# Performance work log

Hardware: AMD Instinct MI355X
Metric: run time of the kernel (lower is better)

The kernel has to match this reference:

```python
import jax, jax.numpy as jnp
import numpy as np
from jax.scipy.stats import norm

N = 6144
D1, D2 = 3000, 1000
H = 128          # hardcoded hidden in VAEEncoder
LAT = 64
E = 16           # num_experts
K = 2            # top-k
NOISE_EPS = 0.01
BN_EPS = 1e-5


def setup_inputs() -> dict:
    key = jax.random.key(0)
    ks = jax.random.split(key, 24)
    xav = lambda k, i, o: jax.random.uniform(k, (i, o), jnp.float32,
                                             -np.sqrt(6.0 / (i + o)), np.sqrt(6.0 / (i + o)))
    u = jax.random.uniform(ks[0], (N, N), jnp.float32)
    adj = u / u.sum(axis=1, keepdims=True)  # row-normalized dense graph
    inp = {
        'x1': jax.random.normal(ks[1], (N, D1), jnp.float32),
        'x2': jax.random.normal(ks[2], (N, D2), jnp.float32),
        'adj': adj,
        # modality-1 VAE encoder
        'W1': xav(ks[3], D1, H), 'gamma1': jnp.ones((H,)), 'beta1': jnp.zeros((H,)),
        'Wmu1': xav(ks[4], H, LAT), 'bmu1': jnp.zeros((LAT,)),
        'Wlv1': xav(ks[5], H, LAT), 'blv1': jnp.zeros((LAT,)),
        # modality-2 VAE encoder
        'W2': xav(ks[6], D2, H), 'gamma2': jnp.ones((H,)), 'beta2': jnp.zeros((H,)),
        'Wmu2': xav(ks[7], H, LAT), 'bmu2': jnp.zeros((LAT,)),
        'Wlv2': xav(ks[8], H, LAT), 'blv2': jnp.zeros((LAT,)),
        # MoE gating (torch inits these to zero; small randn gives a non-degenerate baseline)
        'w_gate': 0.02 * jax.random.normal(ks[9], (LAT, E), jnp.float32),
        'w_noise': 0.02 * jax.random.normal(ks[10], (LAT, E), jnp.float32),
        # modality decoders
        'Wd1': xav(ks[11], LAT, LAT), 'Wfc1': xav(ks[12], LAT, D1), 'bfc1': jnp.zeros((D1,)),
        'Wd2': xav(ks[13], LAT, LAT), 'Wfc2': xav(ks[14], LAT, D2), 'bfc2': jnp.zeros((D2,)),
    }
    return inp


def _encode(x, adj, W, gamma, beta, Wmu, bmu, Wlv, blv):
    h = adj @ (x @ W)                                   # [N,H] GNN embed
    mu_b = h.mean(0)
    var_b = h.var(0)
    h = (h - mu_b) / jnp.sqrt(var_b + BN_EPS) * gamma + beta  # BatchNorm1d (train mode)
    return h @ Wmu + bmu, h @ Wlv + blv                 # mu, logvar [N,LAT]


def _cv_squared(v):
    return v.var(ddof=1) / (v.mean() ** 2 + 1e-10)


def _moe_gating(z, w_gate, w_noise, key):
    clean = z @ w_gate                                  # [N,E]
    std = jax.nn.softplus(z @ w_noise) + NOISE_EPS
    noisy = clean + jax.random.normal(key, clean.shape, clean.dtype) * std
    top_vals, top_idx = jax.lax.top_k(noisy, K + 1)     # [N,K+1]
    topk_gates = jax.nn.softmax(top_vals[:, :K], axis=1)
    rows = jnp.arange(z.shape[0])[:, None]
    gates = jnp.zeros_like(clean).at[rows, top_idx[:, :K]].set(topk_gates)
    # differentiable load estimate (prob each expert is in top-k)
    thr_in = top_vals[:, K][:, None]
    thr_out = top_vals[:, K - 1][:, None]
    is_in = noisy > thr_in
    prob = jnp.where(is_in, norm.cdf((clean - thr_in) / std), norm.cdf((clean - thr_out) / std))
    load = prob.sum(0)
    importance = gates.sum(0)
    loss = _cv_squared(importance) + _cv_squared(load)
    return gates, loss


def _decode(z, adj, Wd, Wfc, bfc):
    return (adj @ (z @ Wd)) @ Wfc + bfc                 # Decoder: mm, mm, Linear


def reference(x1, x2, adj,
              W1, gamma1, beta1, Wmu1, bmu1, Wlv1, blv1,
              W2, gamma2, beta2, Wmu2, bmu2, Wlv2, blv2,
              w_gate, w_noise,
              Wd1, Wfc1, bfc1, Wd2, Wfc2, bfc2):
    mu1, lv1 = _encode(x1, adj, W1, gamma1, beta1, Wmu1, bmu1, Wlv1, blv1)
    mu2, lv2 = _encode(x2, adj, W2, gamma2, beta2, Wmu2, bmu2, Wlv2, blv2)
    # Product of Experts over the 2 modalities
    mus = jnp.stack([mu1, mu2], 0)
    lvs = jnp.stack([lv1, lv2], 0)
    var = jnp.exp(lvs) + 1e-8
    T = 1.0 / (var + 1e-8)
    pd_mu = (mus * T).sum(0) / T.sum(0)
    pd_logvar = jnp.log(1.0 / T.sum(0) + 1e-8)
    z = pd_mu
    gates, moe_loss = _moe_gating(z, w_gate, w_noise, jax.random.key(42))
    recon1 = _decode(z, adj, Wd1, Wfc1, bfc1)
    recon2 = _decode(z, adj, Wd2, Wfc2, bfc2)
    return recon1, recon2, pd_mu, pd_logvar, gates, moe_loss
```

## Files before the change

### kernel.cpp

```cpp
#include <hip/hip_runtime.h>
#include <math.h>

#define NR    6144
#define DIM1  3000
#define DIM2  1000
#define HID   128
#define LATD  64
#define NEXP  16

typedef __bf16 bf16x8 __attribute__((ext_vector_type(8)));
typedef float  f32x4  __attribute__((ext_vector_type(4)));

__device__ __forceinline__ unsigned short f2bf_rne(float x) {
  unsigned u = __float_as_uint(x);
  u += 0x7FFFu + ((u >> 16) & 1u);
  return (unsigned short)(u >> 16);
}
__device__ __forceinline__ void split2(float v, unsigned short& h, unsigned short& l) {
  h = f2bf_rne(v);
  float hf = __uint_as_float((unsigned)h << 16);
  l = f2bf_rne(v - hf);
}
__device__ __forceinline__ unsigned cvt_pk_bf16(float a, float b) {
  unsigned r;
  asm("v_cvt_pk_bf16_f32 %0, %1, %2" : "=v"(r) : "v"(a), "v"(b));
  return r;
}

template<bool SPLIT3, bool ATOMIC>
__device__ __forceinline__ void gemm_body3(
    unsigned short* __restrict__ bufA,
    unsigned short* __restrict__ bufB0, unsigned short* __restrict__ bufB1,
    const float* __restrict__ A, const unsigned short* __restrict__ Bblk,
    const float* __restrict__ bias,
    float* __restrict__ C, int N, int lda, int ldc,
    int bm, int bn, int k0, int kend)
{
  const int tid  = threadIdx.x;
  const int lane = tid & 63;
  const int wave = tid >> 6;
  const int wm = wave >> 1, wn = wave & 1;
  const int lrow = lane & 15, kg = lane >> 4;
  const int nsteps = (kend - k0 + 31) >> 5;
  if (nsteps <= 0) return;

  f32x4 acc[4][4];
  #pragma unroll
  for (int f = 0; f < 4; ++f)
    #pragma unroll
    for (int g = 0; g < 4; ++g)
      #pragma unroll
      for (int j = 0; j < 4; ++j) acc[f][g][j] = 0.f;

  const int srow = tid >> 1;
  const int ks   = (tid & 1) * 16;
  const int s0   = (tid & 1) * 2;
  const float* aRow = A + (size_t)(bm + srow) * lda;
  const int rx = srow & 7;
  const int wa0 = srow * 64 + (((s0 + 0) ^ rx) * 8);
  const int wa1 = srow * 64 + (((s0 + 1) ^ rx) * 8);
  const int wa2 = srow * 64 + (((s0 + 4) ^ rx) * 8);
  const int wa3 = srow * 64 + (((s0 + 5) ^ rx) * 8);

  float va[16];

  #define LOAD_A(gk) {                                                  \
    const int kb = (gk) + ks;                                           \
    if (kb + 16 <= kend) {                                              \
      const float4* ap = (const float4*)(aRow + kb);                    \
      float4 f0 = ap[0], f1 = ap[1], f2 = ap[2], f3 = ap[3];            \
      va[0]=f0.x; va[1]=f0.y; va[2]=f0.z; va[3]=f0.w;                   \
      va[4]=f1.x; va[5]=f1.y; va[6]=f1.z; va[7]=f1.w;                   \
      va[8]=f2.x; va[9]=f2.y; va[10]=f2.z; va[11]=f2.w;                 \
      va[12]=f3.x; va[13]=f3.y; va[14]=f3.z; va[15]=f3.w;               \
    } else {                                                            \
      _Pragma("unroll")                                                 \
      for (int i = 0; i < 16; ++i) va[i] = (kb + i < kend) ? aRow[kb + i] : 0.f; \
    }                                                                   \
  }

  #define STAGE_B(gk, dst) {                                            \
    const unsigned short* _src = Bblk + ((size_t)((gk) >> 5)) * 8192 + wave * 2048 + lane * 8; \
    unsigned short* _d = (dst) + wave * 2048;                           \
    __builtin_amdgcn_global_load_lds((const __attribute__((address_space(1))) unsigned int*)(_src),        (__attribute__((address_space(3))) unsigned int*)(_d),        16, 0, 0); \
    __builtin_amdgcn_global_load_lds((const __attribute__((address_space(1))) unsigned int*)(_src + 512),  (__attribute__((address_space(3))) unsigned int*)(_d + 512),  16, 0, 0); \
    __builtin_amdgcn_global_load_lds((const __attribute__((address_space(1))) unsigned int*)(_src + 1024), (__attribute__((address_space(3))) unsigned int*)(_d + 1024), 16, 0, 0); \
    __builtin_amdgcn_global_load_lds((const __attribute__((address_space(1))) unsigned int*)(_src + 1536), (__attribute__((address_space(3))) unsigned int*)(_d + 1536), 16, 0, 0); \
  }

  LOAD_A(k0);
  STAGE_B(k0, bufB0);

  for (int s = 0; s < nsteps; ++s) {
    unsigned short* bCur = (s & 1) ? bufB1 : bufB0;
    unsigned short* bNxt = (s & 1) ? bufB0 : bufB1;

    unsigned hw[8], lw[8];
    #pragma unroll
    for (int i = 0; i < 8; ++i) {
      hw[i] = cvt_pk_bf16(va[2*i], va[2*i+1]);
      if (SPLIT3) {
        const float h0 = __uint_as_float(hw[i] << 16);
        const float h1 = __uint_as_float(hw[i] & 0xFFFF0000u);
        lw[i] = cvt_pk_bf16(va[2*i] - h0, va[2*i+1] - h1);
      } else {
        lw[i] = 0;
      }
    }

    __syncthreads();
    *(uint4*)&bufA[wa0] = make_uint4(hw[0], hw[1], hw[2], hw[3]);
    *(uint4*)&bufA[wa1] = make_uint4(hw[4], hw[5], hw[6], hw[7]);
    if (SPLIT3) {
      *(uint4*)&bufA[wa2] = make_uint4(lw[0], lw[1], lw[2], lw[3]);
      *(uint4*)&bufA[wa3] = make_uint4(lw[4], lw[5], lw[6], lw[7]);
    }
    __syncthreads();

    if (s + 1 < nsteps) {
      LOAD_A(k0 + (s + 1) * 32);
      STAGE_B(k0 + (s + 1) * 32, bNxt);
    }

    bf16x8 afh[4], bfh[4], afl[4], bfl[4];
    #pragma unroll
    for (int f = 0; f < 4; ++f) {
      const int r = wm * 64 + f * 16 + lrow;
      afh[f] = *(const bf16x8*)&bufA[r * 64 + ((kg ^ (r & 7)) * 8)];
      if (SPLIT3) afl[f] = *(const bf16x8*)&bufA[r * 64 + (((4 + kg) ^ (r & 7)) * 8)];
      const int n = wn * 64 + f * 16 + lrow;
      bfh[f] = *(const bf16x8*)&bCur[n * 64 + ((kg ^ (n & 7)) * 8)];
      if (SPLIT3) bfl[f] = *(const bf16x8*)&bCur[n * 64 + (((4 + kg) ^ (n & 7)) * 8)];
    }
    #pragma unroll
    for (int f = 0; f < 4; ++f)
      #pragma unroll
      for (int g = 0; g < 4; ++g) {
        acc[f][g] = __builtin_amdgcn_mfma_f32_16x16x32_bf16(afh[f], bfh[g], acc[f][g], 0, 0, 0);
        if constexpr (SPLIT3) {
          acc[f][g] = __builtin_amdgcn_mfma_f32_16x16x32_bf16(afl[f], bfh[g], acc[f][g], 0, 0, 0);
          acc[f][g] = __builtin_amdgcn_mfma_f32_16x16x32_bf16(afh[f], bfl[g], acc[f][g], 0, 0, 0);
        }
      }
  }
  #undef LOAD_A
  #undef STAGE_B

  #pragma unroll
  for (int f = 0; f < 4; ++f) {
    #pragma unroll
    for (int g = 0; g < 4; ++g) {
      const int row0 = bm + wm * 64 + f * 16 + (lane >> 4) * 4;
      const int col  = bn + wn * 64 + g * 16 + (lane & 15);
      if (col < N) {
        #pragma unroll
        for (int j = 0; j < 4; ++j) {
          const size_t idx = (size_t)(row0 + j) * ldc + col;
          if (ATOMIC) atomicAdd(&C[idx], acc[f][g][j]);
          else        C[idx] = acc[f][g][j] + (bias ? bias[col] : 0.f);
        }
      }
    }
  }
}

template<bool SPLIT3, bool ATOMIC>
__global__ __launch_bounds__(256, 3) void gemm_mfma3(
    const float* __restrict__ A, const unsigned short* __restrict__ Bblk,
    int kblocks_per_tile, const float* __restrict__ bias, float* __restrict__ C,
    int N, int lda, int ldc, int K, int kchunk)
{
  __shared__ alignas(16) unsigned short bufA[8192];
  __shared__ alignas(16) unsigned short bufB0[8192];
  __shared__ alignas(16) unsigned short bufB1[8192];
  const unsigned short* Bt = Bblk + (size_t)blockIdx.y * kblocks_per_tile * 8192;
  const int k0 = blockIdx.z * kchunk;
  gemm_body3<SPLIT3, ATOMIC>(bufA, bufB0, bufB1, A, Bt, bias, C, N, lda, ldc,
                             blockIdx.x * 128, blockIdx.y * 128, k0, min(k0 + kchunk, K));
}

__global__ __launch_bounds__(256, 3) void gemm_enc3(
    const float* __restrict__ x1, const unsigned short* __restrict__ W1blk,
    const float* __restrict__ x2, const unsigned short* __restrict__ W2blk,
    float* __restrict__ XW)
{
  __shared__ alignas(16) unsigned short bufA[8192];
  __shared__ alignas(16) unsigned short bufB0[8192];
  __shared__ alignas(16) unsigned short bufB1[8192];
  if (blockIdx.y == 0) {
    const int k0 = blockIdx.z * 384;
    gemm_body3<true, true>(bufA, bufB0, bufB1, x1, W1blk, nullptr, XW, HID, DIM1, 256,
                           blockIdx.x * 128, 0, k0, min(k0 + 384, DIM1));
  } else {
    const int k0 = blockIdx.z * 128;
    gemm_body3<true, true>(bufA, bufB0, bufB1, x2, W2blk, nullptr, XW + HID, HID, DIM2, 256,
                           blockIdx.x * 128, 0, k0, min(k0 + 128, DIM2));
  }
}

__global__ __launch_bounds__(256) void pack_b_blocks(
    const float* __restrict__ in, int K, int ldin, int Ncols, int col0,
    unsigned short* __restrict__ out)
{
  __shared__ unsigned short img[8192];
  const int tid = threadIdx.x;
  const int ks  = blockIdx.x;
  const int k0  = ks * 32;
  const int c   = tid & 127;
  const int h   = tid >> 7;
  const int colg = col0 + blockIdx.y * 128 + c;
  #pragma unroll
  for (int i = 0; i < 16; ++i) {
    const int kl = h + 2 * i;
    const int k  = k0 + kl;
    const float v = (k < K && colg < Ncols) ? in[(size_t)k * ldin + colg] : 0.f;
    unsigned short hi, lo;
    split2(v, hi, lo);
    const int base = c * 64 + (kl & 7);
    img[base + (((kl >> 3) ^ (c & 7)) * 8)]       = hi;
    img[base + ((((kl >> 3) + 4) ^ (c & 7)) * 8)] = lo;
  }
  __syncthreads();
  const size_t ob = ((size_t)blockIdx.y * gridDim.x + ks) * 8192;
  const uint4* s4 = (const uint4*)img;
  uint4* o4 = (uint4*)(out + ob);
  #pragma unroll
  for (int i = 0; i < 4; ++i) o4[tid + i * 256] = s4[tid + i * 256];
}

#define BM 64
#define BN 64
#define BK 16

__global__ __launch_bounds__(256) void gemm_f32(
    const float* __restrict__ A, const float* __restrict__ B,
    const float* __restrict__ bias, float* __restrict__ C,
    int M, int N, int K, int lda, int ldb, int ldc)
{
  __shared__ float At[BK][BM + 4];
  __shared__ float Bt[BK][BN + 4];
  const int tid = threadIdx.x;
  const int tx = tid & 15;
  const int ty = tid >> 4;
  const int bm = blockIdx.x * BM;
  const int bn = blockIdx.y * BN;

  float acc[4][4] = {};

  const int ar = tid >> 2;
  const int ak = (tid & 3) * 4;
  const int bk = tid >> 4;
  const int bc = (tid & 15) * 4;

  for (int k0 = 0; k0 < K; k0 += BK) {
    {
      float4 v = make_float4(0.f, 0.f, 0.f, 0.f);
      const int gr = bm + ar;
      const int gk = k0 + ak;
      if (gr < M && gk < K) {
        const float* p = &A[(size_t)gr * lda];
        if (gk + 3 < K) v = *reinterpret_cast<const float4*>(&p[gk]);
        else {
          v.x = p[gk];
          if (gk + 1 < K) v.y = p[gk + 1];
          if (gk + 2 < K) v.z = p[gk + 2];
        }
      }
      At[ak + 0][ar] = v.x; At[ak + 1][ar] = v.y;
      At[ak + 2][ar] = v.z; At[ak + 3][ar] = v.w;
    }
    {
      float4 v = make_float4(0.f, 0.f, 0.f, 0.f);
      const int gk = k0 + bk;
      const int gc = bn + bc;
      if (gk < K) {
        const float* p = &B[(size_t)gk * ldb];
        if (gc + 3 < N) v = *reinterpret_cast<const float4*>(&p[gc]);
        else {
          if (gc     < N) v.x = p[gc];
          if (gc + 1 < N) v.y = p[gc + 1];
          if (gc + 2 < N) v.z = p[gc + 2];
        }
      }
      *reinterpret_cast<float4*>(&Bt[bk][bc]) = v;
    }
    __syncthreads();
    #pragma unroll
    for (int kk = 0; kk < BK; ++kk) {
      float4 a4 = *reinterpret_cast<const float4*>(&At[kk][ty * 4]);
      float4 b4 = *reinterpret_cast<const float4*>(&Bt[kk][tx * 4]);
      float av[4] = {a4.x, a4.y, a4.z, a4.w};
      float bv[4] = {b4.x, b4.y, b4.z, b4.w};
      #pragma unroll
      for (int i = 0; i < 4; ++i)
        #pragma unroll
        for (int j = 0; j < 4; ++j)
          acc[i][j] = fmaf(av[i], bv[j], acc[i][j]);
    }
    __syncthreads();
  }

  #pragma unroll
  for (int i = 0; i < 4; ++i) {
    const int row = bm + ty * 4 + i;
    if (row >= M) continue;
    #pragma unroll
    for (int j = 0; j < 4; ++j) {
      const int col = bn + tx * 4 + j;
      if (col < N) {
        float v = acc[i][j];
        if (bias) v += bias[col];
        C[(size_t)row * ldc + col] = v;
      }
    }
  }
}

__global__ __launch_bounds__(256) void bnstats_kernel(
    const float* __restrict__ H2, float* __restrict__ ssum, float* __restrict__ ssq)
{
  const int c = threadIdx.x;
  const int r0 = blockIdx.x * 12;
  float s = 0.f, q = 0.f;
  #pragma unroll
  for (int i = 0; i < 12; ++i) {
    float v = H2[(size_t)(r0 + i) * 256 + c];
    s += v;
    q = fmaf(v, v, q);
  }
  atomicAdd(&ssum[c], s);
  atomicAdd(&ssq[c], q);
}

__global__ __launch_bounds__(256) void mulv_kernel(
    const float* __restrict__ H2, const float* __restrict__ ssum, const float* __restrict__ ssq,
    const float* __restrict__ g1, const float* __restrict__ b1,
    const float* __restrict__ Wmu1, const float* __restrict__ bmu1,
    const float* __restrict__ Wlv1, const float* __restrict__ blv1,
    const float* __restrict__ g2, const float* __restrict__ b2,
    const float* __restrict__ Wmu2, const float* __restrict__ bmu2,
    const float* __restrict__ Wlv2, const float* __restrict__ blv2,
    float* __restrict__ pd_mu_out, float* __restrict__ pd_lv_out, float* __restrict__ z_out)
{
  __shared__ float hn[4][256];
  const int tid = threadIdx.x;
  const int r0 = blockIdx.x * 4;

  for (int idx = tid; idx < 1024; idx += 256) {
    const int rr = idx >> 8;
    const int c  = idx & 255;
    const float mean = ssum[c] * (1.0f / 6144.0f);
    const float var  = ssq[c] * (1.0f / 6144.0f) - mean * mean;
    const float rstd = 1.0f / sqrtf(var + 1e-5f);
    const float gamma = (c < HID) ? g1[c] : g2[c - HID];
    const float beta  = (c < HID) ? b1[c] : b2[c - HID];
    const float v = H2[(size_t)(r0 + rr) * 256 + c];
    hn[rr][c] = (v - mean) * rstd * gamma + beta;
  }
  __syncthreads();

  const int rr = tid >> 6;
  const int j  = tid & 63;
  float mu1 = bmu1[j], lv1 = blv1[j], mu2 = bmu2[j], lv2 = blv2[j];
  #pragma unroll 4
  for (int k = 0; k < HID; ++k) {
    const float h1 = hn[rr][k];
    const float h2 = hn[rr][HID + k];
    mu1 = fmaf(h1, Wmu1[k * LATD + j], mu1);
    lv1 = fmaf(h1, Wlv1[k * LATD + j], lv1);
    mu2 = fmaf(h2, Wmu2[k * LATD + j], mu2);
    lv2 = fmaf(h2, Wlv2[k * LATD + j], lv2);
  }
  const float var1 = expf(lv1) + 1e-8f;
  const float var2 = expf(lv2) + 1e-8f;
  const float T1 = 1.0f / (var1 + 1e-8f);
  const float T2 = 1.0f / (var2 + 1e-8f);
  const float denom = T1 + T2;
  const float pmu = (mu1 * T1 + mu2 * T2) / denom;
  const float plv = logf(1.0f / denom + 1e-8f);
  const size_t o = (size_t)(r0 + rr) * LATD + j;
  pd_mu_out[o] = pmu;
  pd_lv_out[o] = plv;
  z_out[o]     = pmu;
}

__device__ __forceinline__ unsigned rotl32(unsigned x, int r) {
  return (x << r) | (x >> (32 - r));
}

__device__ float threefry_normal(unsigned i) {
  const unsigned ks0 = 0u;
  const unsigned ks1 = 42u;
  const unsigned ks2 = 0x1BD11BDAu ^ 0u ^ 42u;
  unsigned x0 = 0u + ks0;
  unsigned x1 = i + ks1;

  #define TF_ROUND(r) { x0 += x1; x1 = rotl32(x1, r); x1 ^= x0; }
  TF_ROUND(13) TF_ROUND(15) TF_ROUND(26) TF_ROUND(6)
  x0 += ks1; x1 += ks2 + 1u;
  TF_ROUND(17) TF_ROUND(29) TF_ROUND(16) TF_ROUND(24)
  x0 += ks2; x1 += ks0 + 2u;
  TF_ROUND(13) TF_ROUND(15) TF_ROUND(26) TF_ROUND(6)
  x0 += ks0; x1 += ks1 + 3u;
  TF_ROUND(17) TF_ROUND(29) TF_ROUND(16) TF_ROUND(24)
  x0 += ks1; x1 += ks2 + 4u;
  TF_ROUND(13) TF_ROUND(15) TF_ROUND(26) TF_ROUND(6)
  x0 += ks2; x1 += ks0 + 5u;
  #undef TF_ROUND

  const unsigned bits = x0 ^ x1;

  const unsigned fb = (bits >> 9) | 0x3F800000u;
  const float u01 = __uint_as_float(fb) - 1.0f;
  const float minval = -0.99999994f;
  float u = fmaf(u01, 2.0f, minval);
  u = fmaxf(minval, u);

  float w = -log1pf(-u * u);
  float p;
  if (w < 5.0f) {
    w = w - 2.5f;
    p = 2.81022636e-08f;
    p = fmaf(p, w, 3.43273939e-07f);
    p = fmaf(p, w, -3.5233877e-06f);
    p = fmaf(p, w, -4.39150654e-06f);
    p = fmaf(p, w, 0.00021858087f);
    p = fmaf(p, w, -0.00125372503f);
    p = fmaf(p, w, -0.00417768164f);
    p = fmaf(p, w, 0.246640727f);
    p = fmaf(p, w, 1.50140941f);
  } else {
    w = sqrtf(w) - 3.0f;
    p = -0.000200214257f;
    p = fmaf(p, w, 0.000100950558f);
    p = fmaf(p, w, 0.00134934322f);
    p = fmaf(p, w, -0.00367342844f);
    p = fmaf(p, w, 0.00573950773f);
    p = fmaf(p, w, -0.0076224613f);
    p = fmaf(p, w, 0.00943887047f);
    p = fmaf(p, w, 1.00167406f);
    p = fmaf(p, w, 2.83297682f);
  }
  return 1.4142135f * (p * u);
}

__global__ __launch_bounds__(64) void gating_kernel(
    const float* __restrict__ z, const float* __restrict__ w_gate,
    const float* __restrict__ w_noise, float* __restrict__ gates_out,
    float* __restrict__ importance, float* __restrict__ loadv)
{
  __shared__ float zt[64][65];
  __shared__ float wg[64][16];
  __shared__ float wn[64][16];
  __shared__ float imp_s[16];
  __shared__ float load_s[16];

  const int tid = threadIdx.x;
  const int r0 = blockIdx.x * 64;

  for (int idx = tid; idx < 1024; idx += 64) {
    wg[idx >> 4][idx & 15] = w_gate[idx];
    wn[idx >> 4][idx & 15] = w_noise[idx];
  }
  for (int idx = tid; idx < 4096; idx += 64) {
    const int rr = idx >> 6, c = idx & 63;
    zt[rr][c] = z[(size_t)(r0 + rr) * 64 + c];
  }
  if (tid < 16) { imp_s[tid] = 0.f; load_s[tid] = 0.f; }
  __syncthreads();

  const int r = r0 + tid;
  float clean[16], noisy[16], stdv[16];
  #pragma unroll
  for (int e = 0; e < NEXP; ++e) {
    float c = 0.f, n = 0.f;
    #pragma unroll 8
    for (int k = 0; k < 64; ++k) {
      const float zv = zt[tid][k];
      c = fmaf(zv, wg[k][e], c);
      n = fmaf(zv, wn[k][e], n);
    }
    clean[e] = c;
    const float sp = fmaxf(n, 0.f) + log1pf(expf(-fabsf(n)));
    stdv[e] = sp + 0.01f;
    const float eps = threefry_normal((unsigned)r * 16u + (unsigned)e);
    noisy[e] = fmaf(eps, stdv[e], c);
  }

  float v0 = -1e30f, v1 = -1e30f, v2 = -1e30f;
  int i0 = 0, i1 = 0;
  #pragma unroll
  for (int e = 0; e < NEXP; ++e) {
    const float v = noisy[e];
    if (v > v0)      { v2 = v1; v1 = v0; i1 = i0; v0 = v; i0 = e; }
    else if (v > v1) { v2 = v1; v1 = v; i1 = e; }
    else if (v > v2) { v2 = v; }
  }

  const float e1 = expf(v1 - v0);
  const float inv = 1.0f / (1.0f + e1);
  const float g0 = inv;
  const float g1v = e1 * inv;

  float lacc[16];
  #pragma unroll
  for (int e = 0; e < NEXP; ++e) {
    const float gv = (e == i0) ? g0 : ((e == i1) ? g1v : 0.f);
    gates_out[(size_t)r * NEXP + e] = gv;
    const float thr = (noisy[e] > v2) ? v2 : v1;
    const float x = (clean[e] - thr) / stdv[e];
    lacc[e] = 0.5f * erfcf(-0.70710678f * x);
  }
  atomicAdd(&imp_s[i0], g0);
  atomicAdd(&imp_s[i1], g1v);
  #pragma unroll
  for (int e = 0; e < NEXP; ++e) atomicAdd(&load_s[e], lacc[e]);
  __syncthreads();
  if (tid < 16) {
    atomicAdd(&importance[tid], imp_s[tid]);
    atomicAdd(&loadv[tid], load_s[tid]);
  }
}

__global__ void loss_kernel(const float* __restrict__ imp, const float* __restrict__ ld,
                            float* __restrict__ out)
{
  if (threadIdx.x == 0 && blockIdx.x == 0) {
    float mi = 0.f, ml = 0.f;
    for (int e = 0; e < NEXP; ++e) { mi += imp[e]; ml += ld[e]; }
    mi *= (1.0f / 16.0f);
    ml *= (1.0f / 16.0f);
    float vi = 0.f, vl = 0.f;
    for (int e = 0; e < NEXP; ++e) {
      const float di = imp[e] - mi;
      const float dl = ld[e] - ml;
      vi = fmaf(di, di, vi);
      vl = fmaf(dl, dl, vl);
    }
    vi *= (1.0f / 15.0f);
    vl *= (1.0f / 15.0f);
    out[0] = vi / (mi * mi + 1e-10f) + vl / (ml * ml + 1e-10f);
  }
}

extern "C" void kernel_launch(void* const* d_in, const int* in_sizes, int n_in,
                              void* d_out, int out_size, void* d_ws, size_t ws_size,
                              hipStream_t stream)
{
  const float* x1     = (const float*)d_in[0];
  const float* x2     = (const float*)d_in[1];
  const float* adj    = (const float*)d_in[2];
  const float* W1     = (const float*)d_in[3];
  const float* gamma1 = (const float*)d_in[4];
  const float* beta1  = (const float*)d_in[5];
  const float* Wmu1   = (const float*)d_in[6];
  const float* bmu1   = (const float*)d_in[7];
  const float* Wlv1   = (const float*)d_in[8];
  const float* blv1   = (const float*)d_in[9];
  const float* W2     = (const float*)d_in[10];
  const float* gamma2 = (const float*)d_in[11];
  const float* beta2  = (const float*)d_in[12];
  const float* Wmu2   = (const float*)d_in[13];
  const float* bmu2   = (const float*)d_in[14];
  const float* Wlv2   = (const float*)d_in[15];
  const float* blv2   = (const float*)d_in[16];
  const float* w_gate = (const float*)d_in[17];
  const float* w_noise= (const float*)d_in[18];
  const float* Wd1    = (const float*)d_in[19];
  const float* Wfc1   = (const float*)d_in[20];
  const float* bfc1   = (const float*)d_in[21];
  const float* Wd2    = (const float*)d_in[22];
  const float* Wfc2   = (const float*)d_in[23];
  const float* bfc2   = (const float*)d_in[24];

  float* out = (float*)d_out;
  float* recon1 = out;
  float* recon2 = out + (size_t)NR * DIM1;
  float* pd_mu  = recon2 + (size_t)NR * DIM2;
  float* pd_lv  = pd_mu + (size_t)NR * LATD;
  float* gates  = pd_lv + (size_t)NR * LATD;
  float* loss   = gates + (size_t)NR * NEXP;

  char* wsb = (char*)d_ws;
  const size_t o_XW   = 0;
  const size_t o_H2   = o_XW   + 6291456;
  const size_t o_z    = o_H2   + 6291456;
  const size_t o_ZD   = o_z    + 1572864;
  const size_t o_AZ   = o_ZD   + 3145728;
  const size_t o_XWB  = o_AZ   + 3145728;
  const size_t o_W1B  = o_XWB  + 6291456;
  const size_t o_W2B  = o_W1B  + 1540096;
  const size_t o_stat = o_W2B  + 524288;
  const size_t need   = o_stat + 2176;

  const dim3 blk(256);

  if (ws_size >= need) {
    float* XW   = (float*)(wsb + o_XW);
    float* H2   = (float*)(wsb + o_H2);
    float* zbuf = (float*)(wsb + o_z);
    float* ZD   = (float*)(wsb + o_ZD);
    float* AZ   = (float*)(wsb + o_AZ);
    unsigned short* XWB  = (unsigned short*)(wsb + o_XWB);
    unsigned short* ZDB  = XWB;
    unsigned short* W1B  = (unsigned short*)(wsb + o_W1B);
    unsigned short* W2B  = (unsigned short*)(wsb + o_W2B);
    unsigned short* F1B  = W1B;
    unsigned short* F2B  = W2B;
    float* ssum = (float*)(wsb + o_stat);
    float* ssq  = ssum + 256;
    float* imp  = ssq + 256;
    float* ldv  = imp + 16;

    hipMemsetAsync(XW, 0, 6291456 * 2, stream);
    hipMemsetAsync(AZ, 0, 3145728, stream);
    hipMemsetAsync(ssum, 0, 2176, stream);

    pack_b_blocks<<<dim3(94, 1), blk, 0, stream>>>(W1, DIM1, HID, HID, 0, W1B);
    pack_b_blocks<<<dim3(32, 1), blk, 0, stream>>>(W2, DIM2, HID, HID, 0, W2B);

    gemm_enc3<<<dim3(48, 2, 8), blk, 0, stream>>>(x1, W1B, x2, W2B, XW);

    pack_b_blocks<<<dim3(192, 2), blk, 0, stream>>>(XW, NR, 256, 256, 0, XWB);

    gemm_mfma3<true, true><<<dim3(48, 2, 8), blk, 0, stream>>>(
        adj, XWB, 192, nullptr, H2, 256, NR, 256, NR, 768);

    bnstats_kernel<<<512, blk, 0, stream>>>(H2, ssum, ssq);
    mulv_kernel<<<NR / 4, blk, 0, stream>>>(H2, ssum, ssq,
        gamma1, beta1, Wmu1, bmu1, Wlv1, blv1,
        gamma2, beta2, Wmu2, bmu2, Wlv2, blv2,
        pd_mu, pd_lv, zbuf);

    gating_kernel<<<NR / 64, 64, 0, stream>>>(zbuf, w_gate, w_noise, gates, imp, ldv);
    loss_kernel<<<1, 64, 0, stream>>>(imp, ldv, loss);

    gemm_f32<<<dim3(96, 1), blk, 0, stream>>>(zbuf, Wd1, nullptr, ZD,        NR, LATD, LATD, LATD, LATD, 128);
    gemm_f32<<<dim3(96, 1), blk, 0, stream>>>(zbuf, Wd2, nullptr, ZD + LATD, NR, LATD, LATD, LATD, LATD, 128);

    pack_b_blocks<<<dim3(192, 1), blk, 0, stream>>>(ZD, NR, 128, 128, 0, ZDB);
    gemm_mfma3<false, true><<<dim3(48, 1, 16), blk, 0, stream>>>(
        adj, ZDB, 192, nullptr, AZ, 128, NR, 128, NR, 384);

    pack_b_blocks<<<dim3(2, 24), blk, 0, stream>>>(Wfc1, LATD, DIM1, DIM1, 0, F1B);
    pack_b_blocks<<<dim3(2, 8),  blk, 0, stream>>>(Wfc2, LATD, DIM2, DIM2, 0, F2B);

    gemm_mfma3<false, false><<<dim3(48, 24, 1), blk, 0, stream>>>(
        AZ, F1B, 2, bfc1, recon1, DIM1, 128, DIM1, LATD, 64);
    gemm_mfma3<false, false><<<dim3(48, 8, 1), blk, 0, stream>>>(
        AZ + LATD, F2B, 2, bfc2, recon2, DIM2, 128, DIM2, LATD, 64);
    return;
  }

  float* ws   = (float*)d_ws;
  float* XW   = ws;
  float* H2   = ws + 1572864;
  float* zbuf = ws + 3145728;
  float* ZD   = ws + 3538944;
  float* AZ   = ws + 4325376;
  float* ssum = ws + 5111808;
  float* ssq  = ws + 5112064;
  float* imp  = ws + 5112320;
  float* ldv  = ws + 5112336;

  hipMemsetAsync(ssum, 0, 544 * sizeof(float), stream);

  gemm_f32<<<dim3(NR / BM, 2), blk, 0, stream>>>(x1, W1, nullptr, XW,        NR, HID, DIM1, DIM1, HID, 256);
  gemm_f32<<<dim3(NR / BM, 2), blk, 0, stream>>>(x2, W2, nullptr, XW + HID,  NR, HID, DIM2, DIM2, HID, 256);
  gemm_f32<<<dim3(NR / BM, 4), blk, 0, stream>>>(adj, XW, nullptr, H2, NR, 256, NR, NR, 256, 256);
  bnstats_kernel<<<512, blk, 0, stream>>>(H2, ssum, ssq);
  mulv_kernel<<<NR / 4, blk, 0, stream>>>(H2, ssum, ssq,
                                          gamma1, beta1, Wmu1, bmu1, Wlv1, blv1,
                                          gamma2, beta2, Wmu2, bmu2, Wlv2, blv2,
                                          pd_mu, pd_lv, zbuf);
  gating_kernel<<<NR / 64, 64, 0, stream>>>(zbuf, w_gate, w_noise, gates, imp, ldv);
  loss_kernel<<<1, 64, 0, stream>>>(imp, ldv, loss);
  gemm_f32<<<dim3(NR / BM, 1), blk, 0, stream>>>(zbuf, Wd1, nullptr, ZD,        NR, LATD, LATD, LATD, LATD, 128);
  gemm_f32<<<dim3(NR / BM, 1), blk, 0, stream>>>(zbuf, Wd2, nullptr, ZD + LATD, NR, LATD, LATD, LATD, LATD, 128);
  gemm_f32<<<dim3(NR / BM, 2), blk, 0, stream>>>(adj, ZD, nullptr, AZ, NR, 128, NR, NR, 128, 128);
  gemm_f32<<<dim3(NR / BM, (DIM1 + BN - 1) / BN), blk, 0, stream>>>(AZ,        Wfc1, bfc1, recon1, NR, DIM1, LATD, 128, DIM1, DIM1);
  gemm_f32<<<dim3(NR / BM, (DIM2 + BN - 1) / BN), blk, 0, stream>>>(AZ + LATD, Wfc2, bfc2, recon2, NR, DIM2, LATD, 128, DIM2, DIM2);
}
```

Before: 431.2 us.

## Pack B operands in MFMA fragment order and load directly to registers

Replaces the tile-shaped B packing and LDS double-buffered staging with a fragment-ordered packed layout that each wave reads straight from global memory into registers. This removes two 16 KB LDS buffers per block and the associated LDS reads. It allows more occupancy, at the cost of losing the async prefetch overlap for B and exposing global load latency inside the loop. The A path still goes through LDS as before.

```diff
diff --git a/kernel.cpp b/kernel.cpp
--- a/kernel.cpp
+++ b/kernel.cpp
@@ -28,10 +28,10 @@
 }
 
 template<bool SPLIT3, bool ATOMIC>
-__device__ __forceinline__ void gemm_body3(
+__device__ __forceinline__ void gemm_bodyD(
     unsigned short* __restrict__ bufA,
-    unsigned short* __restrict__ bufB0, unsigned short* __restrict__ bufB1,
-    const float* __restrict__ A, const unsigned short* __restrict__ Bblk,
+    const float* __restrict__ A,
+    const unsigned short* __restrict__ Bpk, int nks, int ntile0,
     const float* __restrict__ bias,
     float* __restrict__ C, int N, int lda, int ldc,
     int bm, int bn, int k0, int kend)
@@ -61,6 +61,9 @@
   const int wa1 = srow * 64 + (((s0 + 1) ^ rx) * 8);
   const int wa2 = srow * 64 + (((s0 + 4) ^ rx) * 8);
   const int wa3 = srow * 64 + (((s0 + 5) ^ rx) * 8);
+
+  const unsigned short* pBbase =
+      Bpk + ((size_t)(ntile0 + wn * 4) * nks + (k0 >> 5)) * 1024 + lane * 8;
 
   float va[16];
 
@@ -79,22 +82,9 @@
     }                                                                   \
   }
 
-  #define STAGE_B(gk, dst) {                                            \
-    const unsigned short* _src = Bblk + ((size_t)((gk) >> 5)) * 8192 + wave * 2048 + lane * 8; \
-    unsigned short* _d = (dst) + wave * 2048;                           \
-    __builtin_amdgcn_global_load_lds((const __attribute__((address_space(1))) unsigned int*)(_src),        (__attribute__((address_space(3))) unsigned int*)(_d),        16, 0, 0); \
-    __builtin_amdgcn_global_load_lds((const __attribute__((address_space(1))) unsigned int*)(_src + 512),  (__attribute__((address_space(3))) unsigned int*)(_d + 512),  16, 0, 0); \
-    __builtin_amdgcn_global_load_lds((const __attribute__((address_space(1))) unsigned int*)(_src + 1024), (__attribute__((address_space(3))) unsigned int*)(_d + 1024), 16, 0, 0); \
-    __builtin_amdgcn_global_load_lds((const __attribute__((address_space(1))) unsigned int*)(_src + 1536), (__attribute__((address_space(3))) unsigned int*)(_d + 1536), 16, 0, 0); \
-  }
-
   LOAD_A(k0);
-  STAGE_B(k0, bufB0);
 
   for (int s = 0; s < nsteps; ++s) {
-    unsigned short* bCur = (s & 1) ? bufB1 : bufB0;
-    unsigned short* bNxt = (s & 1) ? bufB0 : bufB1;
-
     unsigned hw[8], lw[8];
     #pragma unroll
     for (int i = 0; i < 8; ++i) {
@@ -117,20 +107,22 @@
     }
     __syncthreads();
 
-    if (s + 1 < nsteps) {
-      LOAD_A(k0 + (s + 1) * 32);
-      STAGE_B(k0 + (s + 1) * 32, bNxt);
-    }
-
-    bf16x8 afh[4], bfh[4], afl[4], bfl[4];
+    bf16x8 bfh[4], bfl[4];
+    #pragma unroll
+    for (int g = 0; g < 4; ++g) {
+      const unsigned short* p = pBbase + ((size_t)g * nks + s) * 1024;
+      bfh[g] = *(const bf16x8*)p;
+      if (SPLIT3) bfl[g] = *(const bf16x8*)(p + 512);
+    }
+
+    if (s + 1 < nsteps) { LOAD_A(k0 + (s + 1) * 32); }
+
+    bf16x8 afh[4], afl[4];
     #pragma unroll
     for (int f = 0; f < 4; ++f) {
       const int r = wm * 64 + f * 16 + lrow;
       afh[f] = *(const bf16x8*)&bufA[r * 64 + ((kg ^ (r & 7)) * 8)];
       if (SPLIT3) afl[f] = *(const bf16x8*)&bufA[r * 64 + (((4 + kg) ^ (r & 7)) * 8)];
-      const int n = wn * 64 + f * 16 + lrow;
-      bfh[f] = *(const bf16x8*)&bCur[n * 64 + ((kg ^ (n & 7)) * 8)];
-      if (SPLIT3) bfl[f] = *(const bf16x8*)&bCur[n * 64 + (((4 + kg) ^ (n & 7)) * 8)];
     }
     #pragma unroll
     for (int f = 0; f < 4; ++f)
@@ -144,7 +136,6 @@
       }
   }
   #undef LOAD_A
-  #undef STAGE_B
 
   #pragma unroll
   for (int f = 0; f < 4; ++f) {
@@ -165,67 +156,63 @@
 }
 
 template<bool SPLIT3, bool ATOMIC>
-__global__ __launch_bounds__(256, 3) void gemm_mfma3(
-    const float* __restrict__ A, const unsigned short* __restrict__ Bblk,
-    int kblocks_per_tile, const float* __restrict__ bias, float* __restrict__ C,
+__global__ __launch_bounds__(256, 3) void gemm_mfmaD(
+    const float* __restrict__ A, const unsigned short* __restrict__ Bpk,
+    int nks, const float* __restrict__ bias, float* __restrict__ C,
     int N, int lda, int ldc, int K, int kchunk)
 {
   __shared__ alignas(16) unsigned short bufA[8192];
-  __shared__ alignas(16) unsigned short bufB0[8192];
-  __shared__ alignas(16) unsigned short bufB1[8192];
-  const unsigned short* Bt = Bblk + (size_t)blockIdx.y * kblocks_per_tile * 8192;
   const int k0 = blockIdx.z * kchunk;
-  gemm_body3<SPLIT3, ATOMIC>(bufA, bufB0, bufB1, A, Bt, bias, C, N, lda, ldc,
-                             blockIdx.x * 128, blockIdx.y * 128, k0, min(k0 + kchunk, K));
-}
-
-__global__ __launch_bounds__(256, 3) void gemm_enc3(
-    const float* __restrict__ x1, const unsigned short* __restrict__ W1blk,
-    const float* __restrict__ x2, const unsigned short* __restrict__ W2blk,
+  gemm_bodyD<SPLIT3, ATOMIC>(bufA, A, Bpk, nks, blockIdx.y * 8, bias, C,
+                             N, lda, ldc,
+                             blockIdx.x * 128, blockIdx.y * 128,
+                             k0, min(k0 + kchunk, K));
+}
+
+__global__ __launch_bounds__(256, 3) void gemm_encD(
+    const float* __restrict__ x1, const unsigned short* __restrict__ W1pk,
+    const float* __restrict__ x2, const unsigned short* __restrict__ W2pk,
     float* __restrict__ XW)
 {
   __shared__ alignas(16) unsigned short bufA[8192];
-  __shared__ alignas(16) unsigned short bufB0[8192];
-  __shared__ alignas(16) unsigned short bufB1[8192];
   if (blockIdx.y == 0) {
     const int k0 = blockIdx.z * 384;
-    gemm_body3<true, true>(bufA, bufB0, bufB1, x1, W1blk, nullptr, XW, HID, DIM1, 256,
+    gemm_bodyD<true, true>(bufA, x1, W1pk, 94, 0, nullptr, XW, HID, DIM1, 256,
                            blockIdx.x * 128, 0, k0, min(k0 + 384, DIM1));
   } else {
     const int k0 = blockIdx.z * 128;
-    gemm_body3<true, true>(bufA, bufB0, bufB1, x2, W2blk, nullptr, XW + HID, HID, DIM2, 256,
+    gemm_bodyD<true, true>(bufA, x2, W2pk, 32, 0, nullptr, XW + HID, HID, DIM2, 256,
                            blockIdx.x * 128, 0, k0, min(k0 + 128, DIM2));
   }
 }
 
-__global__ __launch_bounds__(256) void pack_b_blocks(
-    const float* __restrict__ in, int K, int ldin, int Ncols, int col0,
+__global__ __launch_bounds__(256) void pack_b_frags(
+    const float* __restrict__ in, int K, int ldin, int Ncols, int nks,
     unsigned short* __restrict__ out)
 {
-  __shared__ unsigned short img[8192];
-  const int tid = threadIdx.x;
-  const int ks  = blockIdx.x;
-  const int k0  = ks * 32;
-  const int c   = tid & 127;
-  const int h   = tid >> 7;
-  const int colg = col0 + blockIdx.y * 128 + c;
-  #pragma unroll
-  for (int i = 0; i < 16; ++i) {
-    const int kl = h + 2 * i;
-    const int k  = k0 + kl;
-    const float v = (k < K && colg < Ncols) ? in[(size_t)k * ldin + colg] : 0.f;
-    unsigned short hi, lo;
-    split2(v, hi, lo);
-    const int base = c * 64 + (kl & 7);
-    img[base + (((kl >> 3) ^ (c & 7)) * 8)]       = hi;
-    img[base + ((((kl >> 3) + 4) ^ (c & 7)) * 8)] = lo;
-  }
-  __syncthreads();
-  const size_t ob = ((size_t)blockIdx.y * gridDim.x + ks) * 8192;
-  const uint4* s4 = (const uint4*)img;
-  uint4* o4 = (uint4*)(out + ob);
-  #pragma unroll
-  for (int i = 0; i < 4; ++i) o4[tid + i * 256] = s4[tid + i * 256];
+  const int lane = threadIdx.x & 63;
+  const int sub  = threadIdx.x >> 6;
+  const int t = blockIdx.x;
+  const int s = blockIdx.y * 4 + sub;
+  if (s >= nks) return;
+  const int n  = t * 16 + (lane & 15);
+  const int kb = s * 32 + (lane >> 4) * 8;
+  const bool nv = (n < Ncols);
+  unsigned hw[4], lw[4];
+  #pragma unroll
+  for (int i = 0; i < 4; ++i) {
+    const int ka = kb + 2 * i, kc = ka + 1;
+    const float v0 = (nv && ka < K) ? in[(size_t)ka * ldin + n] : 0.f;
+    const float v1 = (nv && kc < K) ? in[(size_t)kc * ldin + n] : 0.f;
+    unsigned short h0, l0, h1, l1;
+    split2(v0, h0, l0);
+    split2(v1, h1, l1);
+    hw[i] = (unsigned)h0 | ((unsigned)h1 << 16);
+    lw[i] = (unsigned)l0 | ((unsigned)l1 << 16);
+  }
+  unsigned short* cell = out + ((size_t)t * nks + s) * 1024;
+  *(uint4*)(cell + lane * 8)       = make_uint4(hw[0], hw[1], hw[2], hw[3]);
+  *(uint4*)(cell + 512 + lane * 8) = make_uint4(lw[0], lw[1], lw[2], lw[3]);
 }
 
 #define BM 64
@@ -601,12 +588,12 @@
     float* zbuf = (float*)(wsb + o_z);
     float* ZD   = (float*)(wsb + o_ZD);
     float* AZ   = (float*)(wsb + o_AZ);
-    unsigned short* XWB  = (unsigned short*)(wsb + o_XWB);
-    unsigned short* ZDB  = XWB;
-    unsigned short* W1B  = (unsigned short*)(wsb + o_W1B);
-    unsigned short* W2B  = (unsigned short*)(wsb + o_W2B);
-    unsigned short* F1B  = W1B;
-    unsigned short* F2B  = W2B;
+    unsigned short* XWP = (unsigned short*)(wsb + o_XWB);
+    unsigned short* ZDP = XWP;
+    unsigned short* W1P = (unsigned short*)(wsb + o_W1B);
+    unsigned short* W2P = (unsigned short*)(wsb + o_W2B);
+    unsigned short* F1P = W1P;
+    unsigned short* F2P = W2P;
     float* ssum = (float*)(wsb + o_stat);
     float* ssq  = ssum + 256;
     float* imp  = ssq + 256;
@@ -616,15 +603,15 @@
     hipMemsetAsync(AZ, 0, 3145728, stream);
     hipMemsetAsync(ssum, 0, 2176, stream);
 
-    pack_b_blocks<<<dim3(94, 1), blk, 0, stream>>>(W1, DIM1, HID, HID, 0, W1B);
-    pack_b_blocks<<<dim3(32, 1), blk, 0, stream>>>(W2, DIM2, HID, HID, 0, W2B);
-
-    gemm_enc3<<<dim3(48, 2, 8), blk, 0, stream>>>(x1, W1B, x2, W2B, XW);
-
-    pack_b_blocks<<<dim3(192, 2), blk, 0, stream>>>(XW, NR, 256, 256, 0, XWB);
-
-    gemm_mfma3<true, true><<<dim3(48, 2, 8), blk, 0, stream>>>(
-        adj, XWB, 192, nullptr, H2, 256, NR, 256, NR, 768);
+    pack_b_frags<<<dim3(8, 24), blk, 0, stream>>>(W1, DIM1, HID, HID, 94, W1P);
+    pack_b_frags<<<dim3(8, 8),  blk, 0, stream>>>(W2, DIM2, HID, HID, 32, W2P);
+
+    gemm_encD<<<dim3(48, 2, 8), blk, 0, stream>>>(x1, W1P, x2, W2P, XW);
+
+    pack_b_frags<<<dim3(16, 48), blk, 0, stream>>>(XW, NR, 256, 256, 192, XWP);
+
+    gemm_mfmaD<true, true><<<dim3(48, 2, 8), blk, 0, stream>>>(
+        adj, XWP, 192, nullptr, H2, 256, NR, 256, NR, 768);
 
     bnstats_kernel<<<512, blk, 0, stream>>>(H2, ssum, ssq);
     mulv_kernel<<<NR / 4, blk, 0, stream>>>(H2, ssum, ssq,
@@ -638,17 +625,17 @@
     gemm_f32<<<dim3(96, 1), blk, 0, stream>>>(zbuf, Wd1, nullptr, ZD,        NR, LATD, LATD, LATD, LATD, 128);
     gemm_f32<<<dim3(96, 1), blk, 0, stream>>>(zbuf, Wd2, nullptr, ZD + LATD, NR, LATD, LATD, LATD, LATD, 128);
 
-    pack_b_blocks<<<dim3(192, 1), blk, 0, stream>>>(ZD, NR, 128, 128, 0, ZDB);
-    gemm_mfma3<false, true><<<dim3(48, 1, 16), blk, 0, stream>>>(
-        adj, ZDB, 192, nullptr, AZ, 128, NR, 128, NR, 384);
-
-    pack_b_blocks<<<dim3(2, 24), blk, 0, stream>>>(Wfc1, LATD, DIM1, DIM1, 0, F1B);
-    pack_b_blocks<<<dim3(2, 8),  blk, 0, stream>>>(Wfc2, LATD, DIM2, DIM2, 0, F2B);
-
-    gemm_mfma3<false, false><<<dim3(48, 24, 1), blk, 0, stream>>>(
-        AZ, F1B, 2, bfc1, recon1, DIM1, 128, DIM1, LATD, 64);
-    gemm_mfma3<false, false><<<dim3(48, 8, 1), blk, 0, stream>>>(
-        AZ + LATD, F2B, 2, bfc2, recon2, DIM2, 128, DIM2, LATD, 64);
+    pack_b_frags<<<dim3(8, 48), blk, 0, stream>>>(ZD, NR, 128, 128, 192, ZDP);
+    gemm_mfmaD<false, true><<<dim3(48, 1, 16), blk, 0, stream>>>(
+        adj, ZDP, 192, nullptr, AZ, 128, NR, 128, NR, 384);
+
+    pack_b_frags<<<dim3(192, 1), blk, 0, stream>>>(Wfc1, LATD, DIM1, DIM1, 2, F1P);
+    pack_b_frags<<<dim3(64, 1),  blk, 0, stream>>>(Wfc2, LATD, DIM2, DIM2, 2, F2P);
+
+    gemm_mfmaD<false, false><<<dim3(48, 24, 1), blk, 0, stream>>>(
+        AZ, F1P, 2, bfc1, recon1, DIM1, 128, DIM1, LATD, 64);
+    gemm_mfmaD<false, false><<<dim3(48, 8, 1), blk, 0, stream>>>(
+        AZ + LATD, F2P, 2, bfc2, recon2, DIM2, 128, DIM2, LATD, 64);
     return;
   }
 
```

Measured after the change: 415.2 us. 1.04x faster.
